# Optimization experiments

Hardware: AMD Instinct MI355X
Metric: run time of the kernel (lower is better)

The kernel has to match this reference:

```python
import jax, jax.numpy as jnp
import numpy as np

N, E, D, L = 50000, 800000, 128, 2
NEG_SLOPE = 0.2
LN_EPS = 1e-5


def setup_inputs() -> dict:
    key = jax.random.key(0)
    ks = jax.random.split(key, 6)
    scale = 1.0 / np.sqrt(D)
    x = jax.random.normal(ks[0], (N, D), dtype=jnp.float32)
    edge_index = jax.random.randint(ks[1], (2, E), 0, N, dtype=jnp.int64)
    W = jax.random.normal(ks[2], (L, D, D), dtype=jnp.float32) * scale
    att_src = jax.random.normal(ks[3], (L, D), dtype=jnp.float32) * scale
    att_dst = jax.random.normal(ks[4], (L, D), dtype=jnp.float32) * scale
    bias = jnp.zeros((L, D), dtype=jnp.float32)
    gamma = jnp.ones((L, D), dtype=jnp.float32)
    beta = jnp.zeros((L, D), dtype=jnp.float32)
    return {"x": x, "edge_index": edge_index, "W": W, "att_src": att_src,
            "att_dst": att_dst, "bias": bias, "gamma": gamma, "beta": beta}


def reference(x, edge_index, W, att_src, att_dst, bias, gamma, beta):
    # PyG GATConv (heads=1, concat=True, add_self_loops=True), eval mode
    # (attention/feature dropout disabled), followed by residual + LayerNorm.
    n = x.shape[0]
    loops = jnp.arange(n, dtype=edge_index.dtype)
    ei = jnp.concatenate([edge_index, jnp.stack([loops, loops])], axis=1)
    src, dst = ei[0], ei[1]  # messages flow src -> dst
    for l in range(W.shape[0]):
        h = x @ W[l]                              # [N, D]
        a_src = h @ att_src[l]                    # [N]
        a_dst = h @ att_dst[l]                    # [N]
        logit = jax.nn.leaky_relu(a_src[src] + a_dst[dst], NEG_SLOPE)  # [E+N]
        # segment softmax over incoming edges of each dst node
        m = jax.ops.segment_max(logit, dst, num_segments=n)
        e = jnp.exp(logit - m[dst])
        s = jax.ops.segment_sum(e, dst, num_segments=n)
        alpha = e / s[dst]
        msg = h[src] * alpha[:, None]             # [E+N, D]
        x_att = jax.ops.segment_sum(msg, dst, num_segments=n) + bias[l]
        # residual + LayerNorm
        y = x + x_att
        mu = jnp.mean(y, axis=-1, keepdims=True)
        var = jnp.var(y, axis=-1, keepdims=True)
        x = (y - mu) * jax.lax.rsqrt(var + LN_EPS) * gamma[l] + beta[l]
    return x
```

## Files before the change

### kernel.cpp

```cpp
#include <hip/hip_runtime.h>
#include <hip/hip_fp16.h>

#define D 128
#define NSLOPE 0.2f
#define LN_EPS 1e-5f
#define CAP 6144

typedef unsigned int uint;
typedef float f32x4 __attribute__((ext_vector_type(4)));
typedef _Float16 f16x8 __attribute__((ext_vector_type(8)));

__device__ __forceinline__ float leaky(float x) { return x > 0.f ? x : NSLOPE * x; }
__device__ __forceinline__ uint pkh(float a, float b) {
    __half2 h = __floats2half2_rn(a, b);
    return *reinterpret_cast<uint*>(&h);
}
__device__ __forceinline__ float2 h2f(uint u) {
    __half2 h = *reinterpret_cast<__half2*>(&u);
    return __half22float2(h);
}
__device__ __forceinline__ __half2 u2h2(uint u) {
    return *reinterpret_cast<__half2*>(&u);
}

__global__ void k_ginit(int* __restrict__ gcur, int nbuck) {
    int t = threadIdx.x;
    if (t < nbuck) gcur[t] = t * CAP;
}

__global__ __launch_bounds__(256) void k_bucket(const int* __restrict__ ei,
        int* __restrict__ gcur, uint* __restrict__ staging, int e, int nbuck) {
    __shared__ uint pr[4096];
    __shared__ int hist[256], gbase[256], c2[256];
    int t = threadIdx.x;
    int base = blockIdx.x * 4096;
    hist[t] = 0;
    c2[t] = 0;
    int nv = min(4096, e - base);
    for (int j = t; j < nv; j += 256) {
        int i = base + j;
        pr[j] = ((uint)ei[e + i] << 16) | (uint)ei[i];
    }
    __syncthreads();
    for (int j = t; j < nv; j += 256)
        atomicAdd(&hist[pr[j] >> 24], 1);
    __syncthreads();
    if (t < nbuck && hist[t] > 0) gbase[t] = atomicAdd(&gcur[t], hist[t]);
    __syncthreads();
    for (int j = t; j < nv; j += 256) {
        uint p = pr[j];
        int b = p >> 24;
        int pos = atomicAdd(&c2[b], 1);
        staging[gbase[b] + pos] = p;
    }
}

__global__ __launch_bounds__(256) void k_bdeg(const uint* __restrict__ staging,
        const int* __restrict__ gcur, int* __restrict__ deg,
        int* __restrict__ bsum, int n) {
    __shared__ int h[256];
    __shared__ int ws[4];
    int b = blockIdx.x, t = threadIdx.x;
    h[t] = 0;
    __syncthreads();
    int cnt = gcur[b] - b * CAP;
    for (int i = t; i < cnt; i += 256)
        atomicAdd(&h[(staging[b * CAP + i] >> 16) & 255], 1);
    __syncthreads();
    int node = b * 256 + t;
    int s = h[t];
    if (node < n) deg[node] = s;
    #pragma unroll
    for (int off = 32; off; off >>= 1) s += __shfl_xor(s, off);
    if ((t & 63) == 0) ws[t >> 6] = s;
    __syncthreads();
    if (t == 0) bsum[b] = ws[0] + ws[1] + ws[2] + ws[3];
}

__global__ __launch_bounds__(256) void k_rowptr(const int* __restrict__ deg,
        const int* __restrict__ bsum, int* __restrict__ rowptr, int n, int nb) {
    __shared__ int sb[256];
    __shared__ int lds[256];
    int b = blockIdx.x, t = threadIdx.x;
    sb[t] = (t < nb) ? bsum[t] : 0;
    __syncthreads();
    for (int off = 1; off < 256; off <<= 1) {
        int u = (t >= off) ? sb[t - off] : 0;
        __syncthreads();
        sb[t] += u;
        __syncthreads();
    }
    int ebase = (b == 0) ? 0 : sb[b - 1];
    int node = b * 256 + t;
    int d = (node < n) ? deg[node] : 0;
    lds[t] = d;
    __syncthreads();
    for (int off = 1; off < 256; off <<= 1) {
        int u = (t >= off) ? lds[t - off] : 0;
        __syncthreads();
        lds[t] += u;
        __syncthreads();
    }
    if (node < n) rowptr[node] = ebase + lds[t] - d;
    if (b == gridDim.x - 1 && t == 0) rowptr[n] = sb[nb - 1];
}

__global__ __launch_bounds__(256) void k_bfill(const uint* __restrict__ staging,
        const int* __restrict__ gcur, const int* __restrict__ rowptr,
        int* __restrict__ csr, int n) {
    __shared__ int c2[256];
    int b = blockIdx.x, t = threadIdx.x;
    c2[t] = 0;
    __syncthreads();
    int cnt = gcur[b] - b * CAP;
    for (int i = t; i < cnt; i += 256) {
        uint p = staging[b * CAP + i];
        int d = p >> 16;
        int r = atomicAdd(&c2[d & 255], 1);
        csr[rowptr[d] + r] = (int)(p & 0xffffu);
    }
}

__global__ __launch_bounds__(256) void k_wt(const float* __restrict__ W,
                                            uint* __restrict__ wth) {
    __shared__ float T[128][17];
    int t = threadIdx.x;
    int c0 = blockIdx.x * 16;
    #pragma unroll
    for (int pass = 0; pass < 2; ++pass) {
        int k = pass * 64 + (t >> 2);
        int c = (t & 3) * 4;
        float4 v = *(const float4*)&W[k * D + c0 + c];
        T[k][c] = v.x; T[k][c + 1] = v.y; T[k][c + 2] = v.z; T[k][c + 3] = v.w;
    }
    __syncthreads();
    int cw = t >> 4;
    int k0 = (t & 15) * 8;
    uint4 uh;
    uh.x = pkh(T[k0 + 0][cw], T[k0 + 1][cw]);
    uh.y = pkh(T[k0 + 2][cw], T[k0 + 3][cw]);
    uh.z = pkh(T[k0 + 4][cw], T[k0 + 5][cw]);
    uh.w = pkh(T[k0 + 6][cw], T[k0 + 7][cw]);
    *(uint4*)&wth[(c0 + cw) * 64 + (t & 15) * 4] = uh;
}

template <bool F16IN>
__global__ __launch_bounds__(256) void k_gemm2(const float* __restrict__ xf,
        const uint* __restrict__ xh, const uint* __restrict__ wth,
        const float* __restrict__ avs, const float* __restrict__ avd,
        uint* __restrict__ hb, float* __restrict__ asrc, float* __restrict__ adst, int n) {
    __shared__ char XH[64 * 256];
    __shared__ char WH[128 * 256];
    __shared__ float psL[256], pdL[256];

    int t = threadIdx.x;
    int brow = blockIdx.x * 64;
    int rows = min(64, n - brow);

    #pragma unroll
    for (int i = 0; i < 8; ++i) {
        int f = t + 256 * i;
        int row = f >> 5, k4 = f & 31;
        uint2 ph = make_uint2(0u, 0u);
        if (row < rows) {
            if (F16IN) {
                ph = *(const uint2*)&xh[(size_t)(brow + row) * 64 + k4 * 2];
            } else {
                float4 v = *(const float4*)&xf[(size_t)(brow + row) * D + k4 * 4];
                ph = make_uint2(pkh(v.x, v.y), pkh(v.z, v.w));
            }
        }
        int off = row * 256 + k4 * 8;
        int swz = (row & 7) << 4;
        *(uint2*)(XH + (off ^ swz)) = ph;
    }
    #pragma unroll
    for (int i = 0; i < 8; ++i) {
        int f = t + 256 * i;
        int col = f >> 4, j = f & 15;
        uint4 vh = *(const uint4*)&wth[col * 64 + j * 4];
        int off = col * 256 + j * 16;
        int swz = (col & 7) << 4;
        *(uint4*)(WH + (off ^ swz)) = vh;
    }
    __syncthreads();

    int wave = t >> 6, lane = t & 63;
    int l15 = lane & 15, lk = lane >> 4;

    f32x4 acc[4][2];
    #pragma unroll
    for (int rt = 0; rt < 4; ++rt)
        #pragma unroll
        for (int ct = 0; ct < 2; ++ct)
            acc[rt][ct] = (f32x4){0.f, 0.f, 0.f, 0.f};

    #pragma unroll
    for (int ks = 0; ks < 4; ++ks) {
        f16x8 a[4], b[2];
        #pragma unroll
        for (int rt = 0; rt < 4; ++rt) {
            int row = rt * 16 + l15;
            int off = row * 256 + (ks * 32 + lk * 8) * 2;
            int swz = (row & 7) << 4;
            a[rt] = *(const f16x8*)(XH + (off ^ swz));
        }
        #pragma unroll
        for (int ct = 0; ct < 2; ++ct) {
            int col = wave * 32 + ct * 16 + l15;
            int off = col * 256 + (ks * 32 + lk * 8) * 2;
            int swz = (col & 7) << 4;
            b[ct] = *(const f16x8*)(WH + (off ^ swz));
        }
        #pragma unroll
        for (int rt = 0; rt < 4; ++rt)
            #pragma unroll
            for (int ct = 0; ct < 2; ++ct)
                acc[rt][ct] = __builtin_amdgcn_mfma_f32_16x16x32_f16(a[rt], b[ct], acc[rt][ct], 0, 0, 0);
    }

    float avs_lo = avs[wave * 32 + l15], avs_hi = avs[wave * 32 + 16 + l15];
    float avd_lo = avd[wave * 32 + l15], avd_hi = avd[wave * 32 + 16 + l15];
    #pragma unroll
    for (int rt = 0; rt < 4; ++rt) {
        #pragma unroll
        for (int j = 0; j < 4; ++j) {
            float ps = acc[rt][0][j] * avs_lo + acc[rt][1][j] * avs_hi;
            float pd = acc[rt][0][j] * avd_lo + acc[rt][1][j] * avd_hi;
            #pragma unroll
            for (int off = 8; off; off >>= 1) {
                ps += __shfl_xor(ps, off);
                pd += __shfl_xor(pd, off);
            }
            int row = rt * 16 + lk * 4 + j;
            if (l15 == 0) { psL[wave * 64 + row] = ps; pdL[wave * 64 + row] = pd; }
        }
    }
    #pragma unroll
    for (int rt = 0; rt < 4; ++rt) {
        #pragma unroll
        for (int j = 0; j < 4; ++j) {
            int row = rt * 16 + lk * 4 + j;
            if (row < rows)
                hb[(size_t)(brow + row) * 64 + wave * 16 + l15] =
                    pkh(acc[rt][0][j], acc[rt][1][j]);
        }
    }
    __syncthreads();
    if (t < 64 && t < rows) {
        asrc[brow + t] = psL[t] + psL[64 + t] + psL[128 + t] + psL[192 + t];
        adst[brow + t] = pdL[t] + pdL[64 + t] + pdL[128 + t] + pdL[192 + t];
    }
}

template <int MODE>
__global__ __launch_bounds__(256) void k_attn(const float* __restrict__ xf,
        const uint* __restrict__ xh, const uint* __restrict__ hb,
        const float* __restrict__ asrc, const float* __restrict__ adst,
        const int* __restrict__ rowptr, const int* __restrict__ csr,
        const float* __restrict__ bias, const float* __restrict__ gamma,
        const float* __restrict__ beta, float* __restrict__ out,
        uint* __restrict__ outh, int n) {
    int node = blockIdx.x * 4 + (threadIdx.x >> 6);
    if (node >= n) return;
    int lane = threadIdx.x & 63;
    int grp = lane >> 4;
    int sl = lane & 15;
    int base_lo = (sl >> 2) * 32 + (sl & 3) * 4;

    float a_i = adst[node];
    float slg = leaky(asrc[node] + a_i);
    int rs = rowptr[node], re = rowptr[node + 1];

    float m_g, ssum;
    __half2 acch[4];
    if (grp == 0) {
        m_g = slg; ssum = 1.f;
        uint4 q = *(const uint4*)&hb[(size_t)node * 64 + sl * 4];
        acch[0] = u2h2(q.x); acch[1] = u2h2(q.y);
        acch[2] = u2h2(q.z); acch[3] = u2h2(q.w);
    } else {
        m_g = -1e30f; ssum = 0.f;
        __half2 z = __half2half2(__float2half(0.f));
        #pragma unroll
        for (int j = 0; j < 4; ++j) acch[j] = z;
    }

    for (int e = rs; e < re; e += 8) {
        int e0 = e + grp, e1 = e + 4 + grp;
        int c0 = min(e0, re - 1), c1 = min(e1, re - 1);
        int s0 = csr[c0], s1 = csr[c1];
        uint4 q0 = *(const uint4*)&hb[(size_t)s0 * 64 + sl * 4];
        uint4 q1 = *(const uint4*)&hb[(size_t)s1 * 64 + sl * 4];
        float lg0 = (e0 < re) ? leaky(asrc[s0] + a_i) : -1e30f;
        float lg1 = (e1 < re) ? leaky(asrc[s1] + a_i) : -1e30f;
        float nm = fmaxf(m_g, fmaxf(lg0, lg1));
        if (nm > m_g) {
            float sc = __expf(m_g - nm);
            ssum *= sc;
            __half2 sch = __half2half2(__float2half(sc));
            #pragma unroll
            for (int j = 0; j < 4; ++j) acch[j] = __hmul2(acch[j], sch);
            m_g = nm;
        }
        float w0 = (e0 < re) ? __expf(lg0 - nm) : 0.f;
        float w1 = (e1 < re) ? __expf(lg1 - nm) : 0.f;
        ssum += w0 + w1;
        __half2 w0h = __half2half2(__float2half(w0));
        __half2 w1h = __half2half2(__float2half(w1));
        acch[0] = __hfma2(w0h, u2h2(q0.x), acch[0]);
        acch[1] = __hfma2(w0h, u2h2(q0.y), acch[1]);
        acch[2] = __hfma2(w0h, u2h2(q0.z), acch[2]);
        acch[3] = __hfma2(w0h, u2h2(q0.w), acch[3]);
        acch[0] = __hfma2(w1h, u2h2(q1.x), acch[0]);
        acch[1] = __hfma2(w1h, u2h2(q1.y), acch[1]);
        acch[2] = __hfma2(w1h, u2h2(q1.z), acch[2]);
        acch[3] = __hfma2(w1h, u2h2(q1.w), acch[3]);
    }

    float m = m_g;
    #pragma unroll
    for (int off = 16; off <= 32; off <<= 1) m = fmaxf(m, __shfl_xor(m, off));
    float sc = __expf(m_g - m);
    ssum *= sc;
    float acc[8];
    {
        float2 f0 = __half22float2(acch[0]);
        float2 f1 = __half22float2(acch[1]);
        float2 f2 = __half22float2(acch[2]);
        float2 f3 = __half22float2(acch[3]);
        acc[0] = f0.x * sc; acc[1] = f1.x * sc; acc[2] = f2.x * sc; acc[3] = f3.x * sc;
        acc[4] = f0.y * sc; acc[5] = f1.y * sc; acc[6] = f2.y * sc; acc[7] = f3.y * sc;
    }
    #pragma unroll
    for (int off = 16; off <= 32; off <<= 1) {
        ssum += __shfl_xor(ssum, off);
        #pragma unroll
        for (int j = 0; j < 8; ++j) acc[j] += __shfl_xor(acc[j], off);
    }
    float inv = 1.f / ssum;

    float x0, x1, x2, x3, x4, x5, x6, x7;
    if (MODE == 0) {
        float4 xa = *(const float4*)&xf[(size_t)node * D + base_lo];
        float4 xb = *(const float4*)&xf[(size_t)node * D + base_lo + 16];
        x0 = xa.x; x1 = xa.y; x2 = xa.z; x3 = xa.w;
        x4 = xb.x; x5 = xb.y; x6 = xb.z; x7 = xb.w;
    } else {
        uint2 ua = *(const uint2*)&xh[(size_t)node * 64 + (base_lo >> 1)];
        uint2 ub = *(const uint2*)&xh[(size_t)node * 64 + (base_lo >> 1) + 8];
        float2 fa0 = h2f(ua.x), fa1 = h2f(ua.y), fb0 = h2f(ub.x), fb1 = h2f(ub.y);
        x0 = fa0.x; x1 = fa0.y; x2 = fa1.x; x3 = fa1.y;
        x4 = fb0.x; x5 = fb0.y; x6 = fb1.x; x7 = fb1.y;
    }
    float4 ba = *(const float4*)&bias[base_lo];
    float4 bb = *(const float4*)&bias[base_lo + 16];
    float y[8];
    y[0] = x0 + acc[0] * inv + ba.x;
    y[1] = x1 + acc[1] * inv + ba.y;
    y[2] = x2 + acc[2] * inv + ba.z;
    y[3] = x3 + acc[3] * inv + ba.w;
    y[4] = x4 + acc[4] * inv + bb.x;
    y[5] = x5 + acc[5] * inv + bb.y;
    y[6] = x6 + acc[6] * inv + bb.z;
    y[7] = x7 + acc[7] * inv + bb.w;

    float s1 = 0.f, s2 = 0.f;
    #pragma unroll
    for (int j = 0; j < 8; ++j) { s1 += y[j]; s2 += y[j] * y[j]; }
    #pragma unroll
    for (int off = 1; off <= 8; off <<= 1) {
        s1 += __shfl_xor(s1, off);
        s2 += __shfl_xor(s2, off);
    }
    float mu = s1 * (1.f / D);
    float var = s2 * (1.f / D) - mu * mu;
    float rstd = rsqrtf(var + LN_EPS);

    if (grp == 0) {
        float4 ga = *(const float4*)&gamma[base_lo];
        float4 gb = *(const float4*)&gamma[base_lo + 16];
        float4 bta = *(const float4*)&beta[base_lo];
        float4 btb = *(const float4*)&beta[base_lo + 16];
        float o0 = (y[0] - mu) * rstd * ga.x + bta.x;
        float o1 = (y[1] - mu) * rstd * ga.y + bta.y;
        float o2 = (y[2] - mu) * rstd * ga.z + bta.z;
        float o3 = (y[3] - mu) * rstd * ga.w + bta.w;
        float o4 = (y[4] - mu) * rstd * gb.x + btb.x;
        float o5 = (y[5] - mu) * rstd * gb.y + btb.y;
        float o6 = (y[6] - mu) * rstd * gb.z + btb.z;
        float o7 = (y[7] - mu) * rstd * gb.w + btb.w;
        if (MODE == 0) {
            uint2 oa = make_uint2(pkh(o0, o1), pkh(o2, o3));
            uint2 ob = make_uint2(pkh(o4, o5), pkh(o6, o7));
            *(uint2*)&outh[(size_t)node * 64 + (base_lo >> 1)] = oa;
            *(uint2*)&outh[(size_t)node * 64 + (base_lo >> 1) + 8] = ob;
        } else {
            *(float4*)&out[(size_t)node * D + base_lo] = make_float4(o0, o1, o2, o3);
            *(float4*)&out[(size_t)node * D + base_lo + 16] = make_float4(o4, o5, o6, o7);
        }
    }
}

extern "C" void kernel_launch(void* const* d_in, const int* in_sizes, int n_in,
                              void* d_out, int out_size, void* d_ws, size_t ws_size,
                              hipStream_t stream) {
    const float* x       = (const float*)d_in[0];
    const int*   ei      = (const int*)d_in[1];
    const float* W       = (const float*)d_in[2];
    const float* att_src = (const float*)d_in[3];
    const float* att_dst = (const float*)d_in[4];
    const float* bias    = (const float*)d_in[5];
    const float* gamma   = (const float*)d_in[6];
    const float* beta    = (const float*)d_in[7];
    float* out = (float*)d_out;

    const int N = in_sizes[0] / D;
    const int E = in_sizes[1] / 2;
    const int NBUCK = (N + 255) / 256;

    char* base = (char*)d_ws;
    size_t off = 0;
    auto alloc = [&](size_t bytes) {
        char* p = base + off;
        off += (bytes + 255) & ~(size_t)255;
        return p;
    };
    uint*  hb      = (uint*)alloc((size_t)N * 64 * 4);
    uint*  xh16    = (uint*)alloc((size_t)N * 64 * 4);
    float* asrc    = (float*)alloc((size_t)N * 4);
    float* adst    = (float*)alloc((size_t)N * 4);
    int*   deg     = (int*)alloc((size_t)N * 4);
    int*   rowptr  = (int*)alloc((size_t)(N + 1) * 4);
    int*   csr     = (int*)alloc((size_t)E * 4);
    uint*  staging = (uint*)alloc((size_t)NBUCK * CAP * 4);
    int*   gcur    = (int*)alloc((size_t)NBUCK * 4);
    int*   bsum    = (int*)alloc((size_t)NBUCK * 4);
    uint*  wth     = (uint*)alloc((size_t)D * 64 * 4);

    k_ginit<<<1, 256, 0, stream>>>(gcur, NBUCK);
    k_bucket<<<(E + 4095) / 4096, 256, 0, stream>>>(ei, gcur, staging, E, NBUCK);
    k_bdeg<<<NBUCK, 256, 0, stream>>>(staging, gcur, deg, bsum, N);
    k_rowptr<<<NBUCK, 256, 0, stream>>>(deg, bsum, rowptr, N, NBUCK);
    k_bfill<<<NBUCK, 256, 0, stream>>>(staging, gcur, rowptr, csr, N);

    const int nblk_node = (N + 3) / 4;
    const int nblk_gemm = (N + 63) / 64;

    k_wt<<<8, 256, 0, stream>>>(W, wth);
    k_gemm2<false><<<nblk_gemm, 256, 0, stream>>>(x, nullptr, wth, att_src, att_dst,
                                                  hb, asrc, adst, N);
    k_attn<0><<<nblk_node, 256, 0, stream>>>(x, nullptr, hb, asrc, adst, rowptr, csr,
                                             bias, gamma, beta, nullptr, xh16, N);
    k_wt<<<8, 256, 0, stream>>>(W + (size_t)D * D, wth);
    k_gemm2<true><<<nblk_gemm, 256, 0, stream>>>(nullptr, xh16, wth,
                                                 att_src + D, att_dst + D,
                                                 hb, asrc, adst, N);
    k_attn<1><<<nblk_node, 256, 0, stream>>>(nullptr, xh16, hb, asrc, adst, rowptr, csr,
                                             bias + D, gamma + D, beta + D, out, nullptr, N);
}
```

Baseline: 164.5 us.

## Give each node a 16-lane group and fuse CSR build kernels

```diff
diff --git a/kernel.cpp b/kernel.cpp
--- a/kernel.cpp
+++ b/kernel.cpp
@@ -21,11 +21,6 @@
 }
 __device__ __forceinline__ __half2 u2h2(uint u) {
     return *reinterpret_cast<__half2*>(&u);
-}
-
-__global__ void k_ginit(int* __restrict__ gcur, int nbuck) {
-    int t = threadIdx.x;
-    if (t < nbuck) gcur[t] = t * CAP;
 }
 
 __global__ __launch_bounds__(256) void k_bucket(const int* __restrict__ ei,
@@ -45,7 +40,8 @@
     for (int j = t; j < nv; j += 256)
         atomicAdd(&hist[pr[j] >> 24], 1);
     __syncthreads();
-    if (t < nbuck && hist[t] > 0) gbase[t] = atomicAdd(&gcur[t], hist[t]);
+    if (t < nbuck && hist[t] > 0)
+        gbase[t] = t * CAP + atomicAdd(&gcur[t], hist[t]);
     __syncthreads();
     for (int j = t; j < nv; j += 256) {
         uint p = pr[j];
@@ -55,34 +51,17 @@
     }
 }
 
-__global__ __launch_bounds__(256) void k_bdeg(const uint* __restrict__ staging,
-        const int* __restrict__ gcur, int* __restrict__ deg,
-        int* __restrict__ bsum, int n) {
+__global__ __launch_bounds__(256) void k_bfill2(const uint* __restrict__ staging,
+        const int* __restrict__ gcur, int* __restrict__ rowptr,
+        int* __restrict__ csr, int n, int nb) {
+    __shared__ int sb[256];
     __shared__ int h[256];
-    __shared__ int ws[4];
+    __shared__ int lds[256];
+    __shared__ int c2[256];
     int b = blockIdx.x, t = threadIdx.x;
+    sb[t] = (t < nb) ? gcur[t] : 0;
     h[t] = 0;
-    __syncthreads();
-    int cnt = gcur[b] - b * CAP;
-    for (int i = t; i < cnt; i += 256)
-        atomicAdd(&h[(staging[b * CAP + i] >> 16) & 255], 1);
-    __syncthreads();
-    int node = b * 256 + t;
-    int s = h[t];
-    if (node < n) deg[node] = s;
-    #pragma unroll
-    for (int off = 32; off; off >>= 1) s += __shfl_xor(s, off);
-    if ((t & 63) == 0) ws[t >> 6] = s;
-    __syncthreads();
-    if (t == 0) bsum[b] = ws[0] + ws[1] + ws[2] + ws[3];
-}
-
-__global__ __launch_bounds__(256) void k_rowptr(const int* __restrict__ deg,
-        const int* __restrict__ bsum, int* __restrict__ rowptr, int n, int nb) {
-    __shared__ int sb[256];
-    __shared__ int lds[256];
-    int b = blockIdx.x, t = threadIdx.x;
-    sb[t] = (t < nb) ? bsum[t] : 0;
+    c2[t] = 0;
     __syncthreads();
     for (int off = 1; off < 256; off <<= 1) {
         int u = (t >= off) ? sb[t - off] : 0;
@@ -91,8 +70,11 @@
         __syncthreads();
     }
     int ebase = (b == 0) ? 0 : sb[b - 1];
-    int node = b * 256 + t;
-    int d = (node < n) ? deg[node] : 0;
+    int cnt = gcur[b];
+    for (int i = t; i < cnt; i += 256)
+        atomicAdd(&h[(staging[b * CAP + i] >> 16) & 255], 1);
+    __syncthreads();
+    int d = h[t];
     lds[t] = d;
     __syncthreads();
     for (int off = 1; off < 256; off <<= 1) {
@@ -101,23 +83,18 @@
         lds[t] += u;
         __syncthreads();
     }
-    if (node < n) rowptr[node] = ebase + lds[t] - d;
-    if (b == gridDim.x - 1 && t == 0) rowptr[n] = sb[nb - 1];
-}
-
-__global__ __launch_bounds__(256) void k_bfill(const uint* __restrict__ staging,
-        const int* __restrict__ gcur, const int* __restrict__ rowptr,
-        int* __restrict__ csr, int n) {
-    __shared__ int c2[256];
-    int b = blockIdx.x, t = threadIdx.x;
-    c2[t] = 0;
-    __syncthreads();
-    int cnt = gcur[b] - b * CAP;
+    int rp = ebase + lds[t] - d;
+    int node = b * 256 + t;
+    if (node < n) rowptr[node] = rp;
+    if (b == 0 && t == 0) rowptr[n] = sb[nb - 1];
+    __syncthreads();
+    h[t] = rp;
+    __syncthreads();
     for (int i = t; i < cnt; i += 256) {
         uint p = staging[b * CAP + i];
-        int d = p >> 16;
-        int r = atomicAdd(&c2[d & 255], 1);
-        csr[rowptr[d] + r] = (int)(p & 0xffffu);
+        int dn = (p >> 16) & 255;
+        int r = atomicAdd(&c2[dn], 1);
+        csr[h[dn] + r] = (int)(p & 0xffffu);
     }
 }
 
@@ -125,12 +102,15 @@
                                             uint* __restrict__ wth) {
     __shared__ float T[128][17];
     int t = threadIdx.x;
-    int c0 = blockIdx.x * 16;
+    int layer = blockIdx.x >> 3;
+    int c0 = (blockIdx.x & 7) * 16;
+    const float* Wl = W + (size_t)layer * D * D;
+    uint* wl = wth + (size_t)layer * D * 64;
     #pragma unroll
     for (int pass = 0; pass < 2; ++pass) {
         int k = pass * 64 + (t >> 2);
         int c = (t & 3) * 4;
-        float4 v = *(const float4*)&W[k * D + c0 + c];
+        float4 v = *(const float4*)&Wl[k * D + c0 + c];
         T[k][c] = v.x; T[k][c + 1] = v.y; T[k][c + 2] = v.z; T[k][c + 3] = v.w;
     }
     __syncthreads();
@@ -141,7 +121,7 @@
     uh.y = pkh(T[k0 + 2][cw], T[k0 + 3][cw]);
     uh.z = pkh(T[k0 + 4][cw], T[k0 + 5][cw]);
     uh.w = pkh(T[k0 + 6][cw], T[k0 + 7][cw]);
-    *(uint4*)&wth[(c0 + cw) * 64 + (t & 15) * 4] = uh;
+    *(uint4*)&wl[(c0 + cw) * 64 + (t & 15) * 4] = uh;
 }
 
 template <bool F16IN>
@@ -261,39 +241,30 @@
         const float* __restrict__ bias, const float* __restrict__ gamma,
         const float* __restrict__ beta, float* __restrict__ out,
         uint* __restrict__ outh, int n) {
-    int node = blockIdx.x * 4 + (threadIdx.x >> 6);
+    int node = blockIdx.x * 16 + (threadIdx.x >> 4);
     if (node >= n) return;
-    int lane = threadIdx.x & 63;
-    int grp = lane >> 4;
-    int sl = lane & 15;
+    int sl = threadIdx.x & 15;
     int base_lo = (sl >> 2) * 32 + (sl & 3) * 4;
 
     float a_i = adst[node];
     float slg = leaky(asrc[node] + a_i);
     int rs = rowptr[node], re = rowptr[node + 1];
 
-    float m_g, ssum;
+    float m_g = slg, ssum = 1.f;
     __half2 acch[4];
-    if (grp == 0) {
-        m_g = slg; ssum = 1.f;
+    {
         uint4 q = *(const uint4*)&hb[(size_t)node * 64 + sl * 4];
         acch[0] = u2h2(q.x); acch[1] = u2h2(q.y);
         acch[2] = u2h2(q.z); acch[3] = u2h2(q.w);
-    } else {
-        m_g = -1e30f; ssum = 0.f;
-        __half2 z = __half2half2(__float2half(0.f));
-        #pragma unroll
-        for (int j = 0; j < 4; ++j) acch[j] = z;
-    }
-
-    for (int e = rs; e < re; e += 8) {
-        int e0 = e + grp, e1 = e + 4 + grp;
-        int c0 = min(e0, re - 1), c1 = min(e1, re - 1);
-        int s0 = csr[c0], s1 = csr[c1];
+    }
+
+    for (int e = rs; e < re; e += 2) {
+        int c1 = min(e + 1, re - 1);
+        int s0 = csr[e], s1 = csr[c1];
         uint4 q0 = *(const uint4*)&hb[(size_t)s0 * 64 + sl * 4];
         uint4 q1 = *(const uint4*)&hb[(size_t)s1 * 64 + sl * 4];
-        float lg0 = (e0 < re) ? leaky(asrc[s0] + a_i) : -1e30f;
-        float lg1 = (e1 < re) ? leaky(asrc[s1] + a_i) : -1e30f;
+        float lg0 = leaky(asrc[s0] + a_i);
+        float lg1 = (e + 1 < re) ? leaky(asrc[s1] + a_i) : -1e30f;
         float nm = fmaxf(m_g, fmaxf(lg0, lg1));
         if (nm > m_g) {
             float sc = __expf(m_g - nm);
@@ -303,8 +274,8 @@
             for (int j = 0; j < 4; ++j) acch[j] = __hmul2(acch[j], sch);
             m_g = nm;
         }
-        float w0 = (e0 < re) ? __expf(lg0 - nm) : 0.f;
-        float w1 = (e1 < re) ? __expf(lg1 - nm) : 0.f;
+        float w0 = __expf(lg0 - nm);
+        float w1 = (e + 1 < re) ? __expf(lg1 - nm) : 0.f;
         ssum += w0 + w1;
         __half2 w0h = __half2half2(__float2half(w0));
         __half2 w1h = __half2half2(__float2half(w1));
@@ -318,27 +289,16 @@
         acch[3] = __hfma2(w1h, u2h2(q1.w), acch[3]);
     }
 
-    float m = m_g;
-    #pragma unroll
-    for (int off = 16; off <= 32; off <<= 1) m = fmaxf(m, __shfl_xor(m, off));
-    float sc = __expf(m_g - m);
-    ssum *= sc;
+    float inv = 1.f / ssum;
     float acc[8];
     {
         float2 f0 = __half22float2(acch[0]);
         float2 f1 = __half22float2(acch[1]);
         float2 f2 = __half22float2(acch[2]);
         float2 f3 = __half22float2(acch[3]);
-        acc[0] = f0.x * sc; acc[1] = f1.x * sc; acc[2] = f2.x * sc; acc[3] = f3.x * sc;
-        acc[4] = f0.y * sc; acc[5] = f1.y * sc; acc[6] = f2.y * sc; acc[7] = f3.y * sc;
-    }
-    #pragma unroll
-    for (int off = 16; off <= 32; off <<= 1) {
-        ssum += __shfl_xor(ssum, off);
-        #pragma unroll
-        for (int j = 0; j < 8; ++j) acc[j] += __shfl_xor(acc[j], off);
-    }
-    float inv = 1.f / ssum;
+        acc[0] = f0.x * inv; acc[1] = f1.x * inv; acc[2] = f2.x * inv; acc[3] = f3.x * inv;
+        acc[4] = f0.y * inv; acc[5] = f1.y * inv; acc[6] = f2.y * inv; acc[7] = f3.y * inv;
+    }
 
     float x0, x1, x2, x3, x4, x5, x6, x7;
     if (MODE == 0) {
@@ -356,14 +316,14 @@
     float4 ba = *(const float4*)&bias[base_lo];
     float4 bb = *(const float4*)&bias[base_lo + 16];
     float y[8];
-    y[0] = x0 + acc[0] * inv + ba.x;
-    y[1] = x1 + acc[1] * inv + ba.y;
-    y[2] = x2 + acc[2] * inv + ba.z;
-    y[3] = x3 + acc[3] * inv + ba.w;
-    y[4] = x4 + acc[4] * inv + bb.x;
-    y[5] = x5 + acc[5] * inv + bb.y;
-    y[6] = x6 + acc[6] * inv + bb.z;
-    y[7] = x7 + acc[7] * inv + bb.w;
+    y[0] = x0 + acc[0] + ba.x;
+    y[1] = x1 + acc[1] + ba.y;
+    y[2] = x2 + acc[2] + ba.z;
+    y[3] = x3 + acc[3] + ba.w;
+    y[4] = x4 + acc[4] + bb.x;
+    y[5] = x5 + acc[5] + bb.y;
+    y[6] = x6 + acc[6] + bb.z;
+    y[7] = x7 + acc[7] + bb.w;
 
     float s1 = 0.f, s2 = 0.f;
     #pragma unroll
@@ -377,28 +337,26 @@
     float var = s2 * (1.f / D) - mu * mu;
     float rstd = rsqrtf(var + LN_EPS);
 
-    if (grp == 0) {
-        float4 ga = *(const float4*)&gamma[base_lo];
-        float4 gb = *(const float4*)&gamma[base_lo + 16];
-        float4 bta = *(const float4*)&beta[base_lo];
-        float4 btb = *(const float4*)&beta[base_lo + 16];
-        float o0 = (y[0] - mu) * rstd * ga.x + bta.x;
-        float o1 = (y[1] - mu) * rstd * ga.y + bta.y;
-        float o2 = (y[2] - mu) * rstd * ga.z + bta.z;
-        float o3 = (y[3] - mu) * rstd * ga.w + bta.w;
-        float o4 = (y[4] - mu) * rstd * gb.x + btb.x;
-        float o5 = (y[5] - mu) * rstd * gb.y + btb.y;
-        float o6 = (y[6] - mu) * rstd * gb.z + btb.z;
-        float o7 = (y[7] - mu) * rstd * gb.w + btb.w;
-        if (MODE == 0) {
-            uint2 oa = make_uint2(pkh(o0, o1), pkh(o2, o3));
-            uint2 ob = make_uint2(pkh(o4, o5), pkh(o6, o7));
-            *(uint2*)&outh[(size_t)node * 64 + (base_lo >> 1)] = oa;
-            *(uint2*)&outh[(size_t)node * 64 + (base_lo >> 1) + 8] = ob;
-        } else {
-            *(float4*)&out[(size_t)node * D + base_lo] = make_float4(o0, o1, o2, o3);
-            *(float4*)&out[(size_t)node * D + base_lo + 16] = make_float4(o4, o5, o6, o7);
-        }
+    float4 ga = *(const float4*)&gamma[base_lo];
+    float4 gb = *(const float4*)&gamma[base_lo + 16];
+    float4 bta = *(const float4*)&beta[base_lo];
+    float4 btb = *(const float4*)&beta[base_lo + 16];
+    float o0 = (y[0] - mu) * rstd * ga.x + bta.x;
+    float o1 = (y[1] - mu) * rstd * ga.y + bta.y;
+    float o2 = (y[2] - mu) * rstd * ga.z + bta.z;
+    float o3 = (y[3] - mu) * rstd * ga.w + bta.w;
+    float o4 = (y[4] - mu) * rstd * gb.x + btb.x;
+    float o5 = (y[5] - mu) * rstd * gb.y + btb.y;
+    float o6 = (y[6] - mu) * rstd * gb.z + btb.z;
+    float o7 = (y[7] - mu) * rstd * gb.w + btb.w;
+    if (MODE == 0) {
+        uint2 oa = make_uint2(pkh(o0, o1), pkh(o2, o3));
+        uint2 ob = make_uint2(pkh(o4, o5), pkh(o6, o7));
+        *(uint2*)&outh[(size_t)node * 64 + (base_lo >> 1)] = oa;
+        *(uint2*)&outh[(size_t)node * 64 + (base_lo >> 1) + 8] = ob;
+    } else {
+        *(float4*)&out[(size_t)node * D + base_lo] = make_float4(o0, o1, o2, o3);
+        *(float4*)&out[(size_t)node * D + base_lo + 16] = make_float4(o4, o5, o6, o7);
     }
 }
 
@@ -430,30 +388,25 @@
     uint*  xh16    = (uint*)alloc((size_t)N * 64 * 4);
     float* asrc    = (float*)alloc((size_t)N * 4);
     float* adst    = (float*)alloc((size_t)N * 4);
-    int*   deg     = (int*)alloc((size_t)N * 4);
     int*   rowptr  = (int*)alloc((size_t)(N + 1) * 4);
     int*   csr     = (int*)alloc((size_t)E * 4);
     uint*  staging = (uint*)alloc((size_t)NBUCK * CAP * 4);
     int*   gcur    = (int*)alloc((size_t)NBUCK * 4);
-    int*   bsum    = (int*)alloc((size_t)NBUCK * 4);
-    uint*  wth     = (uint*)alloc((size_t)D * 64 * 4);
-
-    k_ginit<<<1, 256, 0, stream>>>(gcur, NBUCK);
+    uint*  wth     = (uint*)alloc((size_t)2 * D * 64 * 4);
+
+    hipMemsetAsync(gcur, 0, (size_t)NBUCK * 4, stream);
     k_bucket<<<(E + 4095) / 4096, 256, 0, stream>>>(ei, gcur, staging, E, NBUCK);
-    k_bdeg<<<NBUCK, 256, 0, stream>>>(staging, gcur, deg, bsum, N);
-    k_rowptr<<<NBUCK, 256, 0, stream>>>(deg, bsum, rowptr, N, NBUCK);
-    k_bfill<<<NBUCK, 256, 0, stream>>>(staging, gcur, rowptr, csr, N);
-
-    const int nblk_node = (N + 3) / 4;
+    k_bfill2<<<NBUCK, 256, 0, stream>>>(staging, gcur, rowptr, csr, N, NBUCK);
+    k_wt<<<16, 256, 0, stream>>>(W, wth);
+
+    const int nblk_node = (N + 15) / 16;
     const int nblk_gemm = (N + 63) / 64;
 
-    k_wt<<<8, 256, 0, stream>>>(W, wth);
     k_gemm2<false><<<nblk_gemm, 256, 0, stream>>>(x, nullptr, wth, att_src, att_dst,
                                                   hb, asrc, adst, N);
     k_attn<0><<<nblk_node, 256, 0, stream>>>(x, nullptr, hb, asrc, adst, rowptr, csr,
                                              bias, gamma, beta, nullptr, xh16, N);
-    k_wt<<<8, 256, 0, stream>>>(W + (size_t)D * D, wth);
-    k_gemm2<true><<<nblk_gemm, 256, 0, stream>>>(nullptr, xh16, wth,
+    k_gemm2<true><<<nblk_gemm, 256, 0, stream>>>(nullptr, xh16, wth + (size_t)D * 64,
                                                  att_src + D, att_dst + D,
                                                  hb, asrc, adst, N);
     k_attn<1><<<nblk_node, 256, 0, stream>>>(nullptr, xh16, hb, asrc, adst, rowptr, csr,
```

Result: faster. 145.8 us (-11.4%).
